# Kernel tuning notes

Measured on AMD Instinct MI355X. Metric: run time of the kernel, lower is better.

The kernel has to match this reference:

```python
import jax, jax.numpy as jnp
import numpy as np

H = 512

def setup_inputs() -> dict:
    key = jax.random.key(0)
    k1, k2, k3, k4, k5 = jax.random.split(key, 5)
    B, T, S = 8, 256, 256
    encoder_outputs = jax.random.normal(k1, (B, S, H), dtype=jnp.float32)
    query = jax.random.normal(k2, (B, T, H), dtype=jnp.float32)
    mask = jnp.ones((B, S), dtype=bool)
    scale = 1.0 / np.sqrt(H)
    W_h = jax.random.normal(k3, (H, H), dtype=jnp.float32) * scale
    W_s = jax.random.normal(k4, (H, H), dtype=jnp.float32) * scale
    v = jax.random.normal(k5, (H,), dtype=jnp.float32) * scale
    return {"encoder_outputs": encoder_outputs, "query": query, "mask": mask,
            "W_h": W_h, "W_s": W_s, "v": v}

def reference(encoder_outputs, query, mask, W_h, W_s, v):
    # Projections (nn.Linear applies x @ W.T)
    eh = jnp.einsum('bsh,gh->bsg', encoder_outputs, W_h)  # [B,S,H]
    qs = jnp.einsum('bth,gh->btg', query, W_s)            # [B,T,H]
    # Additive score: tanh of broadcast sum -> [B,T,S,H], reduce H via v
    score = jnp.einsum('btsh,h->bts', jnp.tanh(eh[:, None, :, :] + qs[:, :, None, :]), v)
    score = jnp.where(mask[:, None, :], score, -jnp.inf)  # mask src positions
    attn_weights = jax.nn.softmax(score, axis=-1)          # [B,T,S]
    context = jnp.einsum('bts,bsh->bth', attn_weights, encoder_outputs)  # [B,T,H]
    return context
```

## Files before the change

### kernel.cpp

```cpp
#include <hip/hip_runtime.h>
#include <hip/hip_fp16.h>

#define NH 512
#define NS 256
#define NT 256

static constexpr float K2LOG2E = 2.8853900817779268f;

__device__ __forceinline__ float e2(float x) { return __builtin_amdgcn_exp2f(K2LOG2E * x); }
#define RCP(x) __builtin_amdgcn_rcpf(x)

__device__ __forceinline__ unsigned short bf16r(float x) {
    unsigned u = __float_as_uint(x);
    u += 0x7FFFu + ((u >> 16) & 1u);
    return (unsigned short)(u >> 16);
}

using bf16x8 = __attribute__((ext_vector_type(8))) short;
using f32x4  = __attribute__((ext_vector_type(4))) float;

__device__ __forceinline__ void split8(const float4& x, const float4& y,
                                       bf16x8& h8, bf16x8& l8) {
    const float v[8] = {x.x, x.y, x.z, x.w, y.x, y.y, y.z, y.w};
    #pragma unroll
    for (int i = 0; i < 8; ++i) {
        const unsigned short hs = bf16r(v[i]);
        h8[i] = (short)hs;
        l8[i] = (short)bf16r(v[i] - __uint_as_float(((unsigned)hs) << 16));
    }
}

__device__ __forceinline__ void unpack8(const uint4& u, float* f) {
    *(float2*)(f + 0) = __half22float2(*(const __half2*)&u.x);
    *(float2*)(f + 2) = __half22float2(*(const __half2*)&u.y);
    *(float2*)(f + 4) = __half22float2(*(const __half2*)&u.z);
    *(float2*)(f + 6) = __half22float2(*(const __half2*)&u.w);
}

__global__ __launch_bounds__(256, 4)
void proj_mfma_kernel(const float* __restrict__ enc, const float* __restrict__ qry,
                      const float* __restrict__ Wh, const float* __restrict__ Ws,
                      __half* __restrict__ Et16, float* __restrict__ Qbuf,
                      __half* __restrict__ enc16)
{
    const int gemm = blockIdx.z;
    const float* __restrict__ A = gemm ? qry : enc;
    const float* __restrict__ W = gemm ? Ws : Wh;
    const int n0 = blockIdx.x << 6;
    const int m0 = blockIdx.y << 5;

    __shared__ __align__(16) short lds[7680];

    const int tid = threadIdx.x;
    const int wrow = tid >> 2, wck = (tid & 3) << 3;
    const float* Wp = W + (size_t)(n0 + wrow) * NH + wck;
    const int wlws = 2560 + wrow * 40 + wck;

    const bool doA = (tid < 128);
    const int arow = (tid >> 2) & 31, ack = wck;
    const float* Ap = A + (size_t)(m0 + arow) * NH + ack;
    const int alws = arow * 40 + ack;

    float4 pw0 = *(const float4*)(Wp);
    float4 pw1 = *(const float4*)(Wp + 4);
    float4 pa0, pa1;
    if (doA) { pa0 = *(const float4*)(Ap); pa1 = *(const float4*)(Ap + 4); }

    const bool doEnc16 = (gemm == 0) && (n0 == 0);

    const int wv = tid >> 6, lane = tid & 63;
    const int mh = wv & 1, nh = wv >> 1;
    const int lr = lane & 15, qd = lane >> 4;
    const int aoff = ((mh << 4) + lr) * 40 + (qd << 3);
    int woff[2];
    woff[0] = 2560 + ((nh << 5) + lr) * 40 + (qd << 3);
    woff[1] = 2560 + ((nh << 5) + 16 + lr) * 40 + (qd << 3);

    f32x4 acc[2] = {};

    for (int kc = 0; kc < 16; ++kc) {
        bf16x8 swh, swl, sah, sal;
        split8(pw0, pw1, swh, swl);
        if (doA) {
            split8(pa0, pa1, sah, sal);
            if (doEnc16) {
                __half h8[8];
                h8[0] = __float2half(pa0.x); h8[1] = __float2half(pa0.y);
                h8[2] = __float2half(pa0.z); h8[3] = __float2half(pa0.w);
                h8[4] = __float2half(pa1.x); h8[5] = __float2half(pa1.y);
                h8[6] = __float2half(pa1.z); h8[7] = __float2half(pa1.w);
                *(uint4*)(enc16 + (size_t)(m0 + arow) * NH + (kc << 5) + ack) = *(const uint4*)h8;
            }
        }
        __syncthreads();
        *(bf16x8*)&lds[wlws]        = swh;
        *(bf16x8*)&lds[wlws + 2560] = swl;
        if (doA) {
            *(bf16x8*)&lds[alws]        = sah;
            *(bf16x8*)&lds[alws + 1280] = sal;
        }
        __syncthreads();
        if (kc < 15) {
            const int d = (kc + 1) << 5;
            pw0 = *(const float4*)(Wp + d);
            pw1 = *(const float4*)(Wp + d + 4);
            if (doA) {
                pa0 = *(const float4*)(Ap + d);
                pa1 = *(const float4*)(Ap + d + 4);
            }
        }
        const bf16x8 ah = *(const bf16x8*)&lds[aoff];
        const bf16x8 al = *(const bf16x8*)&lds[aoff + 1280];
        #pragma unroll
        for (int ni = 0; ni < 2; ++ni) {
            const bf16x8 wh8 = *(const bf16x8*)&lds[woff[ni]];
            const bf16x8 wl8 = *(const bf16x8*)&lds[woff[ni] + 2560];
            acc[ni] = __builtin_amdgcn_mfma_f32_16x16x32_bf16(ah, wh8, acc[ni], 0, 0, 0);
            acc[ni] = __builtin_amdgcn_mfma_f32_16x16x32_bf16(ah, wl8, acc[ni], 0, 0, 0);
            acc[ni] = __builtin_amdgcn_mfma_f32_16x16x32_bf16(al, wh8, acc[ni], 0, 0, 0);
        }
    }

    if (gemm == 0) {
        const int b_ = m0 >> 8;
        const int sb = (m0 & 255) + (mh << 4) + (qd << 2);
        #pragma unroll
        for (int ni = 0; ni < 2; ++ni) {
            const int hg = (n0 >> 3) + (nh << 2) + (ni << 1) + (lr >> 3);
            const int h7 = lr & 7;
            __half* p = Et16 + (((size_t)(b_ << 6) + hg) << 11)
                             + ((size_t)sb << 3) + h7;
            const f32x4 A4 = acc[ni];
            #pragma unroll
            for (int r = 0; r < 4; ++r) {
                float arg = K2LOG2E * A4[r];
                arg = fminf(fmaxf(arg, -14.0f), 15.5f);
                p[r << 3] = __float2half(__builtin_amdgcn_exp2f(arg));
            }
        }
    } else {
        #pragma unroll
        for (int ni = 0; ni < 2; ++ni) {
            const int h = n0 + (nh << 5) + (ni << 4) + lr;
            const int m = m0 + (mh << 4) + (qd << 2);
            const f32x4 A4 = acc[ni];
            #pragma unroll
            for (int r = 0; r < 4; ++r)
                Qbuf[(size_t)(m + r) * NH + h] = e2(A4[r]);
        }
    }
}

__global__ __launch_bounds__(256, 4)
void score_kernel(const float* __restrict__ v, const __half* __restrict__ Et16,
                  const float* __restrict__ Qbuf, float* __restrict__ upart)
{
    const int b   = blockIdx.x & 7;
    const int tq  = (blockIdx.x >> 3) & 63;
    const int hh  = blockIdx.x >> 9;
    const int t0q = tq << 2;
    const int tid = threadIdx.x, wv = tid >> 6, lane = tid & 63;

    __shared__ __align__(16) float Qs[4 * 256];
    __shared__ __align__(16) float vsm[256];

    ((float4*)Qs)[tid] = *(const float4*)(Qbuf + (size_t)(b * NT + t0q + (tid >> 6)) * NH
                                          + (hh << 8) + ((tid & 63) << 2));
    if (tid < 64) ((float4*)vsm)[tid] = *(const float4*)(v + (hh << 8) + (tid << 2));
    __syncthreads();

    const int tp = wv >> 1, sh = wv & 1;
    const int s0 = (sh << 7) + lane, s1 = s0 + 64;
    const float* __restrict__ q0p = &Qs[(tp << 1) << 8];
    const float* __restrict__ q1p = q0p + 256;

    const __half* __restrict__ EtB = Et16 + ((size_t)b << 17)
                                   + ((size_t)(hh << 5) << 11) + ((size_t)s0 << 3);
    float u00 = 0.f, u01 = 0.f, u10 = 0.f, u11 = 0.f;

    #pragma unroll 2
    for (int hc = 0; hc < 16; ++hc) {
        const __half* p = EtB + ((size_t)hc << 12);
        const uint4 ca0 = *(const uint4*)(p);
        const uint4 ca1 = *(const uint4*)(p + 2048);
        const uint4 cb0 = *(const uint4*)(p + 512);
        const uint4 cb1 = *(const uint4*)(p + 2048 + 512);
        float e0[16], e1[16];
        unpack8(ca0, e0); unpack8(ca1, e0 + 8);
        unpack8(cb0, e1); unpack8(cb1, e1 + 8);
        const int hb = hc << 4;
        #pragma unroll
        for (int g = 0; g < 4; ++g) {
            const float4 vv = *(const float4*)&vsm[hb + (g << 2)];
            const float4 qa = *(const float4*)&q0p[hb + (g << 2)];
            const float4 qb = *(const float4*)&q1p[hb + (g << 2)];
            const int k = g << 2;
            u00 = fmaf(vv.x, RCP(fmaf(e0[k+0], qa.x, 1.f)), u00);
            u01 = fmaf(vv.x, RCP(fmaf(e1[k+0], qa.x, 1.f)), u01);
            u10 = fmaf(vv.x, RCP(fmaf(e0[k+0], qb.x, 1.f)), u10);
            u11 = fmaf(vv.x, RCP(fmaf(e1[k+0], qb.x, 1.f)), u11);
            u00 = fmaf(vv.y, RCP(fmaf(e0[k+1], qa.y, 1.f)), u00);
            u01 = fmaf(vv.y, RCP(fmaf(e1[k+1], qa.y, 1.f)), u01);
            u10 = fmaf(vv.y, RCP(fmaf(e0[k+1], qb.y, 1.f)), u10);
            u11 = fmaf(vv.y, RCP(fmaf(e1[k+1], qb.y, 1.f)), u11);
            u00 = fmaf(vv.z, RCP(fmaf(e0[k+2], qa.z, 1.f)), u00);
            u01 = fmaf(vv.z, RCP(fmaf(e1[k+2], qa.z, 1.f)), u01);
            u10 = fmaf(vv.z, RCP(fmaf(e0[k+2], qb.z, 1.f)), u10);
            u11 = fmaf(vv.z, RCP(fmaf(e1[k+2], qb.z, 1.f)), u11);
            u00 = fmaf(vv.w, RCP(fmaf(e0[k+3], qa.w, 1.f)), u00);
            u01 = fmaf(vv.w, RCP(fmaf(e1[k+3], qa.w, 1.f)), u01);
            u10 = fmaf(vv.w, RCP(fmaf(e0[k+3], qb.w, 1.f)), u10);
            u11 = fmaf(vv.w, RCP(fmaf(e1[k+3], qb.w, 1.f)), u11);
        }
    }

    float* up = upart + (((size_t)(hh << 3) + b) * NT + t0q + (tp << 1)) * NS;
    up[s0]      = u00; up[s1]      = u01;
    up[NS + s0] = u10; up[NS + s1] = u11;
}

__global__ __launch_bounds__(256, 4)
void ctx_kernel(const __half* __restrict__ enc16, const float* __restrict__ upart,
                float* __restrict__ out)
{
    const int b  = blockIdx.x & 7;
    const int t0 = (blockIdx.x >> 3) << 1;
    const int tid = threadIdx.x, wv = tid >> 6, lane = tid & 63;

    __shared__ float ush[2][NS];
    __shared__ __align__(16) float wsm_[2][NS];

    {
        const float* u0p = upart + ((size_t)b * NT + t0) * NS;
        const float* u1p = upart + ((size_t)(8 + b) * NT + t0) * NS;
        ush[0][tid] = u0p[tid]      + u1p[tid];
        ush[1][tid] = u0p[NS + tid] + u1p[NS + tid];
    }
    __syncthreads();

    if (wv < 2) {
        const float a0 = ush[wv][lane],       a1 = ush[wv][lane + 64],
                    a2 = ush[wv][lane + 128], a3 = ush[wv][lane + 192];
        float m = fminf(fminf(a0, a1), fminf(a2, a3));
        #pragma unroll
        for (int off = 32; off > 0; off >>= 1) m = fminf(m, __shfl_xor(m, off, 64));
        const float p0 = e2(m - a0), p1 = e2(m - a1), p2 = e2(m - a2), p3 = e2(m - a3);
        float l = (p0 + p1) + (p2 + p3);
        #pragma unroll
        for (int off = 32; off > 0; off >>= 1) l += __shfl_xor(l, off, 64);
        const float li = RCP(l);
        wsm_[wv][lane]       = p0 * li; wsm_[wv][lane + 64]  = p1 * li;
        wsm_[wv][lane + 128] = p2 * li; wsm_[wv][lane + 192] = p3 * li;
    }
    __syncthreads();

    const int tc = wv & 1, hh = wv >> 1;
    const int hbase = (hh << 8) + (lane << 2);
    const __half* __restrict__ eb = enc16 + ((size_t)(b * NS) << 9) + hbase;
    float c0 = 0.f, c1 = 0.f, c2 = 0.f, c3 = 0.f;
    #pragma unroll 2
    for (int s2 = 0; s2 < NS; s2 += 4) {
        const float4 w4 = *(const float4*)&wsm_[tc][s2];
        const float wk[4] = {w4.x, w4.y, w4.z, w4.w};
        #pragma unroll
        for (int k = 0; k < 4; ++k) {
            const uint2 ew = *(const uint2*)(eb + ((size_t)(s2 + k) << 9));
            const float2 f01 = __half22float2(*(const __half2*)&ew.x);
            const float2 f23 = __half22float2(*(const __half2*)&ew.y);
            c0 = fmaf(wk[k], f01.x, c0); c1 = fmaf(wk[k], f01.y, c1);
            c2 = fmaf(wk[k], f23.x, c2); c3 = fmaf(wk[k], f23.y, c3);
        }
    }
    *(float4*)(out + (size_t)(b * NT + t0 + tc) * NH + hbase)
        = make_float4(c0, c1, c2, c3);
}

extern "C" void kernel_launch(void* const* d_in, const int* in_sizes, int n_in,
                              void* d_out, int out_size, void* d_ws, size_t ws_size,
                              hipStream_t stream)
{
    const float* enc = (const float*)d_in[0];
    const float* qry = (const float*)d_in[1];
    const float* Wh  = (const float*)d_in[3];
    const float* Wsm = (const float*)d_in[4];
    const float* v   = (const float*)d_in[5];
    float* out = (float*)d_out;

    float*  Qbuf  = (float*)d_ws;
    __half* Et16  = (__half*)(Qbuf + 1048576);
    __half* enc16 = Et16 + 1048576;
    float*  upart = (float*)(enc16 + 1048576);

    proj_mfma_kernel<<<dim3(8, 64, 2), 256, 0, stream>>>(enc, qry, Wh, Wsm,
                                                         Et16, Qbuf, enc16);
    score_kernel<<<1024, 256, 0, stream>>>(v, Et16, Qbuf, upart);
    ctx_kernel<<<1024, 256, 0, stream>>>(enc16, upart, out);
}
```

Baseline: 153.9 us.

## Fuse score and context kernels into one attention kernel per (b, 4 queries)

Merges the score kernel (previously split across two H halves writing partial sums to global memory) and the softmax/context kernel into a single kernel. Each block now covers the full H range for 4 queries, keeps scores and weights in shared memory, and computes two query rows per wave in the context loop. This removes the upart global round trip and one launch, but halves the grid to 512 blocks with lower occupancy (launch bounds 2) and doubles the serial loop length per block.

```diff
diff --git a/kernel.cpp b/kernel.cpp
--- a/kernel.cpp
+++ b/kernel.cpp
@@ -151,36 +151,39 @@
     }
 }
 
-__global__ __launch_bounds__(256, 4)
-void score_kernel(const float* __restrict__ v, const __half* __restrict__ Et16,
-                  const float* __restrict__ Qbuf, float* __restrict__ upart)
+__global__ __launch_bounds__(256, 2)
+void attn_kernel(const __half* __restrict__ enc16, const float* __restrict__ v,
+                 const __half* __restrict__ Et16, const float* __restrict__ Qbuf,
+                 float* __restrict__ out)
 {
-    const int b   = blockIdx.x & 7;
-    const int tq  = (blockIdx.x >> 3) & 63;
-    const int hh  = blockIdx.x >> 9;
-    const int t0q = tq << 2;
+    const int b  = blockIdx.x & 7;
+    const int t0 = (blockIdx.x >> 3) << 2;
     const int tid = threadIdx.x, wv = tid >> 6, lane = tid & 63;
 
-    __shared__ __align__(16) float Qs[4 * 256];
-    __shared__ __align__(16) float vsm[256];
-
-    ((float4*)Qs)[tid] = *(const float4*)(Qbuf + (size_t)(b * NT + t0q + (tid >> 6)) * NH
-                                          + (hh << 8) + ((tid & 63) << 2));
-    if (tid < 64) ((float4*)vsm)[tid] = *(const float4*)(v + (hh << 8) + (tid << 2));
+    __shared__ __align__(16) float Qs[4 * NH];
+    __shared__ __align__(16) float vsm[NH];
+    __shared__ float us[4][NS];
+    __shared__ __align__(8) float wsm_[NS][4];
+
+    {
+        const float4* qsrc = (const float4*)(Qbuf + (size_t)(b * NT + t0) * NH);
+        ((float4*)Qs)[tid]       = qsrc[tid];
+        ((float4*)Qs)[tid + 256] = qsrc[tid + 256];
+        if (tid < 128) ((float4*)vsm)[tid] = ((const float4*)v)[tid];
+    }
     __syncthreads();
 
     const int tp = wv >> 1, sh = wv & 1;
     const int s0 = (sh << 7) + lane, s1 = s0 + 64;
-    const float* __restrict__ q0p = &Qs[(tp << 1) << 8];
-    const float* __restrict__ q1p = q0p + 256;
-
-    const __half* __restrict__ EtB = Et16 + ((size_t)b << 17)
-                                   + ((size_t)(hh << 5) << 11) + ((size_t)s0 << 3);
+    const float* __restrict__ q0p = &Qs[(tp << 1) * NH];
+    const float* __restrict__ q1p = q0p + NH;
+
+    const __half* __restrict__ Etp = Et16 + ((size_t)b << 17) + ((size_t)s0 << 3);
     float u00 = 0.f, u01 = 0.f, u10 = 0.f, u11 = 0.f;
 
     #pragma unroll 2
-    for (int hc = 0; hc < 16; ++hc) {
-        const __half* p = EtB + ((size_t)hc << 12);
+    for (int hc = 0; hc < 32; ++hc) {
+        const __half* p = Etp + ((size_t)hc << 12);
         const uint4 ca0 = *(const uint4*)(p);
         const uint4 ca1 = *(const uint4*)(p + 2048);
         const uint4 cb0 = *(const uint4*)(p + 512);
@@ -213,34 +216,13 @@
             u11 = fmaf(vv.w, RCP(fmaf(e1[k+3], qb.w, 1.f)), u11);
         }
     }
-
-    float* up = upart + (((size_t)(hh << 3) + b) * NT + t0q + (tp << 1)) * NS;
-    up[s0]      = u00; up[s1]      = u01;
-    up[NS + s0] = u10; up[NS + s1] = u11;
-}
-
-__global__ __launch_bounds__(256, 4)
-void ctx_kernel(const __half* __restrict__ enc16, const float* __restrict__ upart,
-                float* __restrict__ out)
-{
-    const int b  = blockIdx.x & 7;
-    const int t0 = (blockIdx.x >> 3) << 1;
-    const int tid = threadIdx.x, wv = tid >> 6, lane = tid & 63;
-
-    __shared__ float ush[2][NS];
-    __shared__ __align__(16) float wsm_[2][NS];
+    us[(tp << 1) + 0][s0] = u00; us[(tp << 1) + 0][s1] = u01;
+    us[(tp << 1) + 1][s0] = u10; us[(tp << 1) + 1][s1] = u11;
+    __syncthreads();
 
     {
-        const float* u0p = upart + ((size_t)b * NT + t0) * NS;
-        const float* u1p = upart + ((size_t)(8 + b) * NT + t0) * NS;
-        ush[0][tid] = u0p[tid]      + u1p[tid];
-        ush[1][tid] = u0p[NS + tid] + u1p[NS + tid];
-    }
-    __syncthreads();
-
-    if (wv < 2) {
-        const float a0 = ush[wv][lane],       a1 = ush[wv][lane + 64],
-                    a2 = ush[wv][lane + 128], a3 = ush[wv][lane + 192];
+        const float a0 = us[wv][lane],       a1 = us[wv][lane + 64],
+                    a2 = us[wv][lane + 128], a3 = us[wv][lane + 192];
         float m = fminf(fminf(a0, a1), fminf(a2, a3));
         #pragma unroll
         for (int off = 32; off > 0; off >>= 1) m = fminf(m, __shfl_xor(m, off, 64));
@@ -249,30 +231,29 @@
         #pragma unroll
         for (int off = 32; off > 0; off >>= 1) l += __shfl_xor(l, off, 64);
         const float li = RCP(l);
-        wsm_[wv][lane]       = p0 * li; wsm_[wv][lane + 64]  = p1 * li;
-        wsm_[wv][lane + 128] = p2 * li; wsm_[wv][lane + 192] = p3 * li;
+        wsm_[lane      ][wv] = p0 * li; wsm_[lane +  64][wv] = p1 * li;
+        wsm_[lane + 128][wv] = p2 * li; wsm_[lane + 192][wv] = p3 * li;
     }
     __syncthreads();
 
-    const int tc = wv & 1, hh = wv >> 1;
+    const int hh = wv & 1;
     const int hbase = (hh << 8) + (lane << 2);
     const __half* __restrict__ eb = enc16 + ((size_t)(b * NS) << 9) + hbase;
-    float c0 = 0.f, c1 = 0.f, c2 = 0.f, c3 = 0.f;
-    #pragma unroll 2
-    for (int s2 = 0; s2 < NS; s2 += 4) {
-        const float4 w4 = *(const float4*)&wsm_[tc][s2];
-        const float wk[4] = {w4.x, w4.y, w4.z, w4.w};
-        #pragma unroll
-        for (int k = 0; k < 4; ++k) {
-            const uint2 ew = *(const uint2*)(eb + ((size_t)(s2 + k) << 9));
-            const float2 f01 = __half22float2(*(const __half2*)&ew.x);
-            const float2 f23 = __half22float2(*(const __half2*)&ew.y);
-            c0 = fmaf(wk[k], f01.x, c0); c1 = fmaf(wk[k], f01.y, c1);
-            c2 = fmaf(wk[k], f23.x, c2); c3 = fmaf(wk[k], f23.y, c3);
-        }
-    }
-    *(float4*)(out + (size_t)(b * NT + t0 + tc) * NH + hbase)
-        = make_float4(c0, c1, c2, c3);
+    float c00=0.f,c01=0.f,c02=0.f,c03=0.f, c10=0.f,c11=0.f,c12=0.f,c13=0.f;
+    #pragma unroll 4
+    for (int s = 0; s < NS; ++s) {
+        const uint2 ew = *(const uint2*)(eb + ((size_t)s << 9));
+        const float2 f01 = __half22float2(*(const __half2*)&ew.x);
+        const float2 f23 = __half22float2(*(const __half2*)&ew.y);
+        const float2 w2 = *(const float2*)&wsm_[s][tp << 1];
+        c00 = fmaf(w2.x, f01.x, c00); c01 = fmaf(w2.x, f01.y, c01);
+        c02 = fmaf(w2.x, f23.x, c02); c03 = fmaf(w2.x, f23.y, c03);
+        c10 = fmaf(w2.y, f01.x, c10); c11 = fmaf(w2.y, f01.y, c11);
+        c12 = fmaf(w2.y, f23.x, c12); c13 = fmaf(w2.y, f23.y, c13);
+    }
+    float* ob = out + (size_t)(b * NT + t0 + (tp << 1)) * NH + hbase;
+    *(float4*)ob        = make_float4(c00, c01, c02, c03);
+    *(float4*)(ob + NH) = make_float4(c10, c11, c12, c13);
 }
 
 extern "C" void kernel_launch(void* const* d_in, const int* in_sizes, int n_in,
@@ -289,10 +270,8 @@
     float*  Qbuf  = (float*)d_ws;
     __half* Et16  = (__half*)(Qbuf + 1048576);
     __half* enc16 = Et16 + 1048576;
-    float*  upart = (float*)(enc16 + 1048576);
 
     proj_mfma_kernel<<<dim3(8, 64, 2), 256, 0, stream>>>(enc, qry, Wh, Wsm,
                                                          Et16, Qbuf, enc16);
-    score_kernel<<<1024, 256, 0, stream>>>(v, Et16, Qbuf, upart);
-    ctx_kernel<<<1024, 256, 0, stream>>>(enc16, upart, out);
-}
+    attn_kernel<<<512, 256, 0, stream>>>(enc16, v, Et16, Qbuf, out);
+}
```

Result: faster. 145.0 us (-5.8%).
